# Optimization experiments

Hardware: AMD Instinct MI355X
Metric: run time of the kernel (lower is better)

Reference implementation:

```python
import jax, jax.numpy as jnp
import numpy as np

COMMITMENT_COST = 0.25
B, T, D = 32, 2048, 64
K = 1024


def setup_inputs() -> dict:
    key = jax.random.key(0)
    k1, k2 = jax.random.split(key)
    inputs = jax.random.normal(k1, (B, T, D), dtype=jnp.float32)
    # codebook init: uniform(-1/K, 1/K) in the original; use same scale
    embedding = jax.random.uniform(k2, (K, D), dtype=jnp.float32,
                                   minval=-1.0 / K, maxval=1.0 / K)
    return {"inputs": inputs, "embedding": embedding}


def reference(inputs, embedding):
    Bb, Tt, Dd = inputs.shape
    flat = inputs.reshape(-1, Dd)  # [N, D]
    dist = (jnp.sum(flat * flat, axis=1, keepdims=True)
            + jnp.sum(embedding * embedding, axis=1)[None, :]
            - 2.0 * (flat @ embedding.T))
    encoding_indices = jnp.argmin(dist, axis=1)  # [N]
    quantized = embedding[encoding_indices].reshape(Bb, Tt, Dd)
    # commitment loss: mse(stop_grad(quantized), inputs)
    e_latent_loss = jnp.mean((jax.lax.stop_gradient(quantized) - inputs) ** 2)
    vq_loss = COMMITMENT_COST * e_latent_loss
    codebook_loss = jnp.zeros((), dtype=jnp.float32)
    # straight-through estimator
    quantized_st = inputs + jax.lax.stop_gradient(quantized - inputs)
    return (quantized_st, encoding_indices.reshape(Bb, Tt),
            vq_loss, e_latent_loss, codebook_loss)
```

## Files before the change

kernel.cpp:

```cpp
#include <hip/hip_runtime.h>
#include <hip/hip_bf16.h>
#include <math.h>


typedef __attribute__((ext_vector_type(8))) short bf16x8;
typedef __attribute__((ext_vector_type(4))) float f32x4;

namespace {
constexpr int NROWS  = 65536;
constexpr int DDIM   = 64;
constexpr int KCODES = 1024;
constexpr float EPSB = 4e-5f;

constexpr size_t WS_LOSS = 0;
constexpr size_t WS_CNT  = 64;
constexpr size_t WS_SE   = 256;
constexpr size_t WS_EHB  = 8192;
constexpr size_t WS_ELB  = WS_EHB + (size_t)65536 * 2;
constexpr size_t WS_BIDX = WS_ELB + (size_t)65536 * 2;
constexpr size_t WS_LIST = WS_BIDX + (size_t)NROWS * 4;
constexpr size_t WS_KEY  = WS_LIST + (size_t)NROWS * 4;
constexpr size_t WS_MV   = WS_KEY + (size_t)NROWS * 8;
constexpr size_t WS_KV   = WS_MV + (size_t)4 * NROWS * 8;
}

__device__ inline short f2bf(float v) {
  __hip_bfloat16 h = __float2bfloat16(v);
  return *reinterpret_cast<short*>(&h);
}
__device__ inline float bf2f(short s) {
  __hip_bfloat16 h;
  *reinterpret_cast<short*>(&h) = s;
  return __bfloat162float(h);
}
__device__ inline f32x4 mfma16(bf16x8 a, bf16x8 b, f32x4 c) {
  return __builtin_amdgcn_mfma_f32_16x16x32_bf16(a, b, c, 0, 0, 0);
}
__device__ inline unsigned int fflip(unsigned int b) {
  return b ^ ((unsigned int)((int)b >> 31) | 0x80000000u);
}

__global__ __launch_bounds__(256) void vq_prep(const float* __restrict__ emb,
                                               float* __restrict__ se,
                                               short* __restrict__ ehB,
                                               short* __restrict__ elB,
                                               unsigned long long* __restrict__ keyBest,
                                               double* __restrict__ loss_accum,
                                               int* __restrict__ cnt) {
  #pragma clang fp contract(off)
  const int gid = blockIdx.x * 256 + (int)threadIdx.x;
  if (gid == 0) { *loss_accum = 0.0; *cnt = 0; }
  keyBest[gid] = ~0ull;

  if (gid < KCODES) {
    const float* e = emb + (size_t)gid * DDIM;
    float r[8];
    #pragma unroll
    for (int j = 0; j < 8; ++j) r[j] = e[j] * e[j];
    #pragma unroll
    for (int i = 8; i < DDIM; i += 8) {
      #pragma unroll
      for (int j = 0; j < 8; ++j) r[j] += e[i + j] * e[i + j];
    }
    se[gid] = ((r[0] + r[1]) + (r[2] + r[3])) + ((r[4] + r[5]) + (r[6] + r[7]));
  }

  if (gid < 8192) {
    const int t  = gid >> 7;
    const int dc = (gid >> 6) & 1;
    const int l  = gid & 63;
    const int code = t * 16 + (l & 15);
    const int d0   = dc * 32 + (l >> 4) * 8;
    const float* ep = emb + (size_t)code * DDIM + d0;
    const size_t ob = ((size_t)(t * 2 + dc) * 64 + l) * 8;
    #pragma unroll
    for (int i = 0; i < 8; ++i) {
      const float v = ep[i];
      const short h = f2bf(v);
      ehB[ob + i] = h;
      elB[ob + i] = f2bf(v - bf2f(h));
    }
  }
}

__global__ __launch_bounds__(256, 2) void vq_fused(const float* __restrict__ x,
                                                   const short* __restrict__ ehB,
                                                   const short* __restrict__ elB,
                                                   const float* __restrict__ se,
                                                   float2* __restrict__ mv,
                                                   unsigned long long* __restrict__ kv) {
  #pragma clang fp contract(off)
  __shared__ float sel[256];
  const int tid  = (int)threadIdx.x;
  const int l    = tid & 63;
  const int wid  = tid >> 6;
  const int quar = (int)blockIdx.x & 3;
  const int rblk = (int)blockIdx.x >> 2;
  const int t0   = quar * 16;
  sel[tid] = se[t0 * 16 + tid];
  __syncthreads();

  const int wrb = rblk * 128 + wid * 32;
  bf16x8 xh[2][2], xl[2][2];
  #pragma unroll
  for (int rt = 0; rt < 2; ++rt) {
    const float* xp = x + (size_t)(wrb + rt * 16 + (l & 15)) * DDIM + (l >> 4) * 8;
    #pragma unroll
    for (int dc = 0; dc < 2; ++dc) {
      const float4 v0 = *reinterpret_cast<const float4*>(xp + dc * 32);
      const float4 v1 = *reinterpret_cast<const float4*>(xp + dc * 32 + 4);
      const float vv[8] = {v0.x, v0.y, v0.z, v0.w, v1.x, v1.y, v1.z, v1.w};
      #pragma unroll
      for (int i = 0; i < 8; ++i) {
        const short h = f2bf(vv[i]);
        xh[rt][dc][i] = h;
        xl[rt][dc][i] = f2bf(vv[i] - bf2f(h));
      }
    }
  }

  float m1v[2][4], m2v[2][4];
  int   m1t[2][4];
  #pragma unroll
  for (int rt = 0; rt < 2; ++rt)
    #pragma unroll
    for (int r = 0; r < 4; ++r) { m1v[rt][r] = INFINITY; m2v[rt][r] = INFINITY; m1t[rt][r] = 0; }

  const size_t lb = (size_t)l * 8;
#define FRAGLD(buf, tt, half2) \
  (*reinterpret_cast<const bf16x8*>((buf) + (size_t)(tt) * 1024 + (half2) * 512 + lb))

  bf16x8 c0 = FRAGLD(ehB, t0, 0), c1 = FRAGLD(ehB, t0, 1),
         c2 = FRAGLD(elB, t0, 0), c3 = FRAGLD(elB, t0, 1);
  bf16x8 n0 = FRAGLD(ehB, t0 + 1, 0), n1 = FRAGLD(ehB, t0 + 1, 1),
         n2 = FRAGLD(elB, t0 + 1, 0), n3 = FRAGLD(elB, t0 + 1, 1);

  const f32x4 kz = {0.f, 0.f, 0.f, 0.f};
  #pragma unroll 4
  for (int tt = 0; tt < 16; ++tt) {
    const int t = t0 + tt;
    const int tf = (tt + 2 < 16) ? t + 2 : t0 + 15;
    bf16x8 f0 = FRAGLD(ehB, tf, 0), f1 = FRAGLD(ehB, tf, 1),
           f2 = FRAGLD(elB, tf, 0), f3 = FRAGLD(elB, tf, 1);

    f32x4 a0, a1;
    a0 = mfma16(xh[0][0], c0, kz);  a1 = mfma16(xh[1][0], c0, kz);
    a0 = mfma16(xh[0][1], c1, a0);  a1 = mfma16(xh[1][1], c1, a1);
    a0 = mfma16(xh[0][0], c2, a0);  a1 = mfma16(xh[1][0], c2, a1);
    a0 = mfma16(xh[0][1], c3, a0);  a1 = mfma16(xh[1][1], c3, a1);
    a0 = mfma16(xl[0][0], c0, a0);  a1 = mfma16(xl[1][0], c0, a1);
    a0 = mfma16(xl[0][1], c1, a0);  a1 = mfma16(xl[1][1], c1, a1);

    const float sev = sel[tt * 16 + (l & 15)];
    #pragma unroll
    for (int r = 0; r < 4; ++r) {
      {
        const float d = __builtin_fmaf(-2.0f, a0[r], sev);
        const bool c = d < m1v[0][r];
        m2v[0][r] = fminf(m2v[0][r], fmaxf(m1v[0][r], d));
        m1t[0][r] = c ? t : m1t[0][r];
        m1v[0][r] = fminf(m1v[0][r], d);
      }
      {
        const float d = __builtin_fmaf(-2.0f, a1[r], sev);
        const bool c = d < m1v[1][r];
        m2v[1][r] = fminf(m2v[1][r], fmaxf(m1v[1][r], d));
        m1t[1][r] = c ? t : m1t[1][r];
        m1v[1][r] = fminf(m1v[1][r], d);
      }
    }
    c0 = n0; c1 = n1; c2 = n2; c3 = n3;
    n0 = f0; n1 = f1; n2 = f2; n3 = f3;
  }
#undef FRAGLD

  const int colbase = l & 15;
  #pragma unroll
  for (int rt = 0; rt < 2; ++rt) {
    #pragma unroll
    for (int r = 0; r < 4; ++r) {
      float m1 = m1v[rt][r], m2 = m2v[rt][r];
      unsigned long long key =
          ((unsigned long long)fflip(__float_as_uint(m1)) << 32)
          | (unsigned)(m1t[rt][r] * 16 + colbase);
      #pragma unroll
      for (int off = 1; off < 16; off <<= 1) {
        const unsigned long long ok = __shfl_xor(key, off, 16);
        const float om1 = __shfl_xor(m1, off, 16);
        const float om2 = __shfl_xor(m2, off, 16);
        m2 = fminf(fminf(m2, om2), fmaxf(m1, om1));
        m1 = fminf(m1, om1);
        key = (ok < key) ? ok : key;
      }
      if (colbase == 0) {
        const int row = wrb + rt * 16 + (l >> 4) * 4 + r;
        mv[(size_t)quar * NROWS + row] = make_float2(m1, m2);
        kv[(size_t)quar * NROWS + row] = key;
      }
    }
  }
}

__global__ __launch_bounds__(256) void vq_combine(const float2* __restrict__ mv,
                                                  const unsigned long long* __restrict__ kv,
                                                  int* __restrict__ bidx,
                                                  int* __restrict__ list,
                                                  int* __restrict__ cnt) {
  const int gid = blockIdx.x * 256 + (int)threadIdx.x;
  const int l = (int)threadIdx.x & 63;
  const float2 A = mv[gid];
  const float2 B = mv[(size_t)NROWS + gid];
  const float2 C = mv[(size_t)2 * NROWS + gid];
  const float2 D = mv[(size_t)3 * NROWS + gid];
  unsigned long long kg = kv[gid];
  {
    unsigned long long k2 = kv[(size_t)NROWS + gid];     kg = (k2 < kg) ? k2 : kg;
    k2 = kv[(size_t)2 * NROWS + gid];                    kg = (k2 < kg) ? k2 : kg;
    k2 = kv[(size_t)3 * NROWS + gid];                    kg = (k2 < kg) ? k2 : kg;
  }
  const float lo1 = fminf(A.x, B.x), hi1 = fmaxf(A.x, B.x);
  const float lo2 = fminf(C.x, D.x), hi2 = fmaxf(C.x, D.x);
  const float m1g = fminf(lo1, lo2);
  const float sec = fminf(fmaxf(lo1, lo2), fminf(hi1, hi2));
  const float m2g = fminf(sec, fminf(fminf(A.y, B.y), fminf(C.y, D.y)));
  const bool cert = m2g > m1g + EPSB;
  bidx[gid] = cert ? (int)(kg & 0xffffffffull) : -1;

  const unsigned long long mask = __ballot(!cert);
  int base = 0;
  if (l == 0 && mask) base = atomicAdd(cnt, (int)__popcll(mask));
  base = __shfl(base, 0, 64);
  if (!cert) {
    const int off = (int)__popcll(mask & ((1ull << l) - 1ull));
    list[base + off] = gid;
  }
}

__global__ __launch_bounds__(64) void vq_exact(const float* __restrict__ x,
                                               const float* __restrict__ emb,
                                               const float* __restrict__ se,
                                               const int* __restrict__ list,
                                               const int* __restrict__ cnt,
                                               unsigned long long* __restrict__ keyBest) {
  #pragma clang fp contract(off)
  __shared__ __align__(16) float eL[32 * DDIM];
  const int n = *cnt;
  if (n == 0) return;
  const int nrb = (n + 63) >> 6;
  const int ntasks = nrb * 32;
  const int l = (int)threadIdx.x;

  for (int t = (int)blockIdx.x; t < ntasks; t += (int)gridDim.x) {
    const int part = t & 31;
    const int rb   = t >> 5;
    const int j0   = part * 32;

    {
      const float4* src = reinterpret_cast<const float4*>(emb + (size_t)j0 * DDIM);
      float4* dst = reinterpret_cast<float4*>(eL);
      #pragma unroll
      for (int i = 0; i < 8; ++i) dst[i * 64 + l] = src[i * 64 + l];
    }
    __syncthreads();

    const int idx = rb * 64 + l;
    const bool act = idx < n;
    const int row = act ? list[idx] : 0;
    const float4* xr4 = reinterpret_cast<const float4*>(x + (size_t)row * DDIM);

    float xv[DDIM];
    #pragma unroll
    for (int q = 0; q < 16; ++q) {
      const float4 v = xr4[q];
      xv[q * 4 + 0] = v.x; xv[q * 4 + 1] = v.y;
      xv[q * 4 + 2] = v.z; xv[q * 4 + 3] = v.w;
    }

    float rr[8];
    #pragma unroll
    for (int j = 0; j < 8; ++j) rr[j] = xv[j] * xv[j];
    #pragma unroll
    for (int i = 8; i < DDIM; i += 8) {
      #pragma unroll
      for (int j = 0; j < 8; ++j) rr[j] += xv[i + j] * xv[i + j];
    }
    const float sx = ((rr[0] + rr[1]) + (rr[2] + rr[3])) + ((rr[4] + rr[5]) + (rr[6] + rr[7]));

    unsigned long long best = ~0ull;
    #pragma unroll 1
    for (int g = 0; g < 8; ++g) {
      const int jb = g * 4;
      const float4* e0 = reinterpret_cast<const float4*>(eL + (jb + 0) * DDIM);
      const float4* e1 = reinterpret_cast<const float4*>(eL + (jb + 1) * DDIM);
      const float4* e2 = reinterpret_cast<const float4*>(eL + (jb + 2) * DDIM);
      const float4* e3 = reinterpret_cast<const float4*>(eL + (jb + 3) * DDIM);
      float a0 = 0.f, a1 = 0.f, a2 = 0.f, a3 = 0.f;
      #pragma unroll
      for (int q = 0; q < 16; ++q) {
        const float4 v0 = e0[q], v1 = e1[q], v2 = e2[q], v3 = e3[q];
        const float xa = xv[q * 4 + 0], xb = xv[q * 4 + 1];
        const float xc = xv[q * 4 + 2], xd = xv[q * 4 + 3];
        a0 = __builtin_fmaf(xa, v0.x, a0); a0 = __builtin_fmaf(xb, v0.y, a0);
        a0 = __builtin_fmaf(xc, v0.z, a0); a0 = __builtin_fmaf(xd, v0.w, a0);
        a1 = __builtin_fmaf(xa, v1.x, a1); a1 = __builtin_fmaf(xb, v1.y, a1);
        a1 = __builtin_fmaf(xc, v1.z, a1); a1 = __builtin_fmaf(xd, v1.w, a1);
        a2 = __builtin_fmaf(xa, v2.x, a2); a2 = __builtin_fmaf(xb, v2.y, a2);
        a2 = __builtin_fmaf(xc, v2.z, a2); a2 = __builtin_fmaf(xd, v2.w, a2);
        a3 = __builtin_fmaf(xa, v3.x, a3); a3 = __builtin_fmaf(xb, v3.y, a3);
        a3 = __builtin_fmaf(xc, v3.z, a3); a3 = __builtin_fmaf(xd, v3.w, a3);
      }
      const int j = j0 + jb;
      const float T0 = sx + se[j + 0];
      const float T1 = sx + se[j + 1];
      const float T2 = sx + se[j + 2];
      const float T3 = sx + se[j + 3];
      const float di0 = __builtin_fmaf(-2.0f, a0, T0);
      const float di1 = __builtin_fmaf(-2.0f, a1, T1);
      const float di2 = __builtin_fmaf(-2.0f, a2, T2);
      const float di3 = __builtin_fmaf(-2.0f, a3, T3);
      unsigned long long k;
      k = ((unsigned long long)fflip(__float_as_uint(di0)) << 32) | (unsigned)(j + 0);
      best = (k < best) ? k : best;
      k = ((unsigned long long)fflip(__float_as_uint(di1)) << 32) | (unsigned)(j + 1);
      best = (k < best) ? k : best;
      k = ((unsigned long long)fflip(__float_as_uint(di2)) << 32) | (unsigned)(j + 2);
      best = (k < best) ? k : best;
      k = ((unsigned long long)fflip(__float_as_uint(di3)) << 32) | (unsigned)(j + 3);
      best = (k < best) ? k : best;
    }
    if (act) atomicMin(&keyBest[row], best);
    __syncthreads();
  }
}

__global__ __launch_bounds__(256) void vq_finalize(const float* __restrict__ x,
                                                   const float* __restrict__ emb,
                                                   const int* __restrict__ bidx,
                                                   const unsigned long long* __restrict__ keyBest,
                                                   float* __restrict__ out,
                                                   double* __restrict__ loss_accum) {
  #pragma clang fp contract(off)
  __shared__ float wsum[4];
  const int tid = (int)threadIdx.x;
  const int l   = tid & 63;
  const int wid = tid >> 6;
  const int sub = l >> 4;
  const int q16 = l & 15;
  float lacc = 0.f;

  #pragma unroll
  for (int it = 0; it < 4; ++it) {
    const int row = blockIdx.x * 64 + it * 16 + wid * 4 + sub;
    int bi = bidx[row];
    if (bi < 0) bi = (int)(keyBest[row] & 0xffffffffull);
    const float4 xv = reinterpret_cast<const float4*>(x)[(size_t)row * 16 + q16];
    const float4 ev = reinterpret_cast<const float4*>(emb)[(size_t)bi * 16 + q16];
    const float da = ev.x - xv.x;
    const float db = ev.y - xv.y;
    const float dc = ev.z - xv.z;
    const float dd = ev.w - xv.w;
    float4 o;
    o.x = xv.x + da; o.y = xv.y + db; o.z = xv.z + dc; o.w = xv.w + dd;
    reinterpret_cast<float4*>(out)[(size_t)row * 16 + q16] = o;
    lacc += da * da + db * db + dc * dc + dd * dd;
    if (q16 == 0) out[(size_t)NROWS * DDIM + row] = (float)bi;
  }
  #pragma unroll
  for (int off = 32; off > 0; off >>= 1) lacc += __shfl_down(lacc, off, 64);
  if (l == 0) wsum[wid] = lacc;
  __syncthreads();
  if (tid == 0)
    atomicAdd(loss_accum, (double)(wsum[0] + wsum[1] + wsum[2] + wsum[3]));
}

__global__ void vq_scalars(const double* __restrict__ loss_accum,
                           float* __restrict__ out) {
  if (threadIdx.x == 0 && blockIdx.x == 0) {
    const double mm = *loss_accum / (double)((size_t)NROWS * DDIM);
    const float el = (float)mm;
    float* tail = out + (size_t)NROWS * DDIM + NROWS;
    tail[0] = 0.25f * el;
    tail[1] = el;
    tail[2] = 0.0f;
  }
}

extern "C" void kernel_launch(void* const* d_in, const int* in_sizes, int n_in,
                              void* d_out, int out_size, void* d_ws, size_t ws_size,
                              hipStream_t stream) {
  const float* x   = (const float*)d_in[0];
  const float* emb = (const float*)d_in[1];
  float* out = (float*)d_out;
  char* ws = (char*)d_ws;

  double* loss_accum = (double*)(ws + WS_LOSS);
  int*    cnt        = (int*)(ws + WS_CNT);
  float*  se         = (float*)(ws + WS_SE);
  short*  ehB        = (short*)(ws + WS_EHB);
  short*  elB        = (short*)(ws + WS_ELB);
  int*    bidx       = (int*)(ws + WS_BIDX);
  int*    list       = (int*)(ws + WS_LIST);
  unsigned long long* keyBest = (unsigned long long*)(ws + WS_KEY);
  float2* mv         = (float2*)(ws + WS_MV);
  unsigned long long* kv = (unsigned long long*)(ws + WS_KV);

  vq_prep<<<NROWS / 256, 256, 0, stream>>>(emb, se, ehB, elB, keyBest,
                                           loss_accum, cnt);
  vq_fused<<<(NROWS / 128) * 4, 256, 0, stream>>>(x, ehB, elB, se, mv, kv);
  vq_combine<<<NROWS / 256, 256, 0, stream>>>(mv, kv, bidx, list, cnt);
  vq_exact<<<2048, 64, 0, stream>>>(x, emb, se, list, cnt, keyBest);
  vq_finalize<<<NROWS / 64, 256, 0, stream>>>(x, emb, bidx, keyBest, out,
                                              loss_accum);
  vq_scalars<<<1, 64, 0, stream>>>(loss_accum, out);
}
```

Before: 98.73 us.

## Fuse output write into combine kernel; finalize only uncertain rows

The combine kernel now writes the quantized output, index and loss contribution for every row whose approximate argmin is certain, keeping the decisions in shared memory instead of a global bidx array. A small final kernel then processes only the rows listed as uncertain, using the exact-pass result. This removes a full pass that reread x and bidx for all rows, and moves most output writing earlier, before the exact pass. In exchange, the combine kernel becomes heavier and its loop now branches per row on the certainty flag.

```diff
diff --git a/kernel.cpp b/kernel.cpp
--- a/kernel.cpp
+++ b/kernel.cpp
@@ -201,39 +201,79 @@
   }
 }
 
-__global__ __launch_bounds__(256) void vq_combine(const float2* __restrict__ mv,
-                                                  const unsigned long long* __restrict__ kv,
-                                                  int* __restrict__ bidx,
-                                                  int* __restrict__ list,
-                                                  int* __restrict__ cnt) {
-  const int gid = blockIdx.x * 256 + (int)threadIdx.x;
-  const int l = (int)threadIdx.x & 63;
-  const float2 A = mv[gid];
-  const float2 B = mv[(size_t)NROWS + gid];
-  const float2 C = mv[(size_t)2 * NROWS + gid];
-  const float2 D = mv[(size_t)3 * NROWS + gid];
-  unsigned long long kg = kv[gid];
+__global__ __launch_bounds__(256) void vq_combine_out(const float2* __restrict__ mv,
+                                                      const unsigned long long* __restrict__ kv,
+                                                      const float* __restrict__ x,
+                                                      const float* __restrict__ emb,
+                                                      int* __restrict__ list,
+                                                      int* __restrict__ cnt,
+                                                      float* __restrict__ out,
+                                                      double* __restrict__ loss_accum) {
+  #pragma clang fp contract(off)
+  __shared__ int   sbidx[256];
+  __shared__ float wsum[4];
+  const int tid = (int)threadIdx.x;
+  const int gid = blockIdx.x * 256 + tid;
+  const int l   = tid & 63;
+
   {
-    unsigned long long k2 = kv[(size_t)NROWS + gid];     kg = (k2 < kg) ? k2 : kg;
-    k2 = kv[(size_t)2 * NROWS + gid];                    kg = (k2 < kg) ? k2 : kg;
-    k2 = kv[(size_t)3 * NROWS + gid];                    kg = (k2 < kg) ? k2 : kg;
-  }
-  const float lo1 = fminf(A.x, B.x), hi1 = fmaxf(A.x, B.x);
-  const float lo2 = fminf(C.x, D.x), hi2 = fmaxf(C.x, D.x);
-  const float m1g = fminf(lo1, lo2);
-  const float sec = fminf(fmaxf(lo1, lo2), fminf(hi1, hi2));
-  const float m2g = fminf(sec, fminf(fminf(A.y, B.y), fminf(C.y, D.y)));
-  const bool cert = m2g > m1g + EPSB;
-  bidx[gid] = cert ? (int)(kg & 0xffffffffull) : -1;
-
-  const unsigned long long mask = __ballot(!cert);
-  int base = 0;
-  if (l == 0 && mask) base = atomicAdd(cnt, (int)__popcll(mask));
-  base = __shfl(base, 0, 64);
-  if (!cert) {
-    const int off = (int)__popcll(mask & ((1ull << l) - 1ull));
-    list[base + off] = gid;
-  }
+    const float2 A = mv[gid];
+    const float2 B = mv[(size_t)NROWS + gid];
+    const float2 C = mv[(size_t)2 * NROWS + gid];
+    const float2 D = mv[(size_t)3 * NROWS + gid];
+    unsigned long long kg = kv[gid];
+    {
+      unsigned long long k2 = kv[(size_t)NROWS + gid];     kg = (k2 < kg) ? k2 : kg;
+      k2 = kv[(size_t)2 * NROWS + gid];                    kg = (k2 < kg) ? k2 : kg;
+      k2 = kv[(size_t)3 * NROWS + gid];                    kg = (k2 < kg) ? k2 : kg;
+    }
+    const float lo1 = fminf(A.x, B.x), hi1 = fmaxf(A.x, B.x);
+    const float lo2 = fminf(C.x, D.x), hi2 = fmaxf(C.x, D.x);
+    const float m1g = fminf(lo1, lo2);
+    const float sec = fminf(fmaxf(lo1, lo2), fminf(hi1, hi2));
+    const float m2g = fminf(sec, fminf(fminf(A.y, B.y), fminf(C.y, D.y)));
+    const bool cert = m2g > m1g + EPSB;
+    sbidx[tid] = cert ? (int)(kg & 0xffffffffull) : -1;
+
+    const unsigned long long mask = __ballot(!cert);
+    int base = 0;
+    if (l == 0 && mask) base = atomicAdd(cnt, (int)__popcll(mask));
+    base = __shfl(base, 0, 64);
+    if (!cert) {
+      const int off = (int)__popcll(mask & ((1ull << l) - 1ull));
+      list[base + off] = gid;
+    }
+  }
+  __syncthreads();
+
+  const int wid = tid >> 6;
+  const int sub = l >> 4;
+  const int q16 = l & 15;
+  float lacc = 0.f;
+
+  for (int it = 0; it < 16; ++it) {
+    const int rloc = it * 16 + wid * 4 + sub;
+    const int bi = sbidx[rloc];
+    if (bi < 0) continue;
+    const int row = blockIdx.x * 256 + rloc;
+    const float4 xv = reinterpret_cast<const float4*>(x)[(size_t)row * 16 + q16];
+    const float4 ev = reinterpret_cast<const float4*>(emb)[(size_t)bi * 16 + q16];
+    const float da = ev.x - xv.x;
+    const float db = ev.y - xv.y;
+    const float dc = ev.z - xv.z;
+    const float dd = ev.w - xv.w;
+    float4 o;
+    o.x = xv.x + da; o.y = xv.y + db; o.z = xv.z + dc; o.w = xv.w + dd;
+    reinterpret_cast<float4*>(out)[(size_t)row * 16 + q16] = o;
+    lacc += da * da + db * db + dc * dc + dd * dd;
+    if (q16 == 0) out[(size_t)NROWS * DDIM + row] = (float)bi;
+  }
+  #pragma unroll
+  for (int off = 32; off > 0; off >>= 1) lacc += __shfl_down(lacc, off, 64);
+  if (l == 0) wsum[wid] = lacc;
+  __syncthreads();
+  if (tid == 0)
+    atomicAdd(loss_accum, (double)(wsum[0] + wsum[1] + wsum[2] + wsum[3]));
 }
 
 __global__ __launch_bounds__(64) void vq_exact(const float* __restrict__ x,
@@ -333,26 +373,27 @@
   }
 }
 
-__global__ __launch_bounds__(256) void vq_finalize(const float* __restrict__ x,
-                                                   const float* __restrict__ emb,
-                                                   const int* __restrict__ bidx,
-                                                   const unsigned long long* __restrict__ keyBest,
-                                                   float* __restrict__ out,
-                                                   double* __restrict__ loss_accum) {
+__global__ __launch_bounds__(256) void vq_minifinal(const float* __restrict__ x,
+                                                    const float* __restrict__ emb,
+                                                    const int* __restrict__ list,
+                                                    const int* __restrict__ cnt,
+                                                    const unsigned long long* __restrict__ keyBest,
+                                                    float* __restrict__ out,
+                                                    double* __restrict__ loss_accum) {
   #pragma clang fp contract(off)
-  __shared__ float wsum[4];
-  const int tid = (int)threadIdx.x;
-  const int l   = tid & 63;
-  const int wid = tid >> 6;
+  const int n = *cnt;
+  const int l   = (int)threadIdx.x & 63;
   const int sub = l >> 4;
   const int q16 = l & 15;
+  const int w   = blockIdx.x * 4 + ((int)threadIdx.x >> 6);
+  const int nW  = (int)gridDim.x * 4;
   float lacc = 0.f;
 
-  #pragma unroll
-  for (int it = 0; it < 4; ++it) {
-    const int row = blockIdx.x * 64 + it * 16 + wid * 4 + sub;
-    int bi = bidx[row];
-    if (bi < 0) bi = (int)(keyBest[row] & 0xffffffffull);
+  for (int base = w * 4; base < n; base += nW * 4) {
+    const int i = base + sub;
+    if (i >= n) continue;
+    const int row = list[i];
+    const int bi = (int)(keyBest[row] & 0xffffffffull);
     const float4 xv = reinterpret_cast<const float4*>(x)[(size_t)row * 16 + q16];
     const float4 ev = reinterpret_cast<const float4*>(emb)[(size_t)bi * 16 + q16];
     const float da = ev.x - xv.x;
@@ -367,10 +408,7 @@
   }
   #pragma unroll
   for (int off = 32; off > 0; off >>= 1) lacc += __shfl_down(lacc, off, 64);
-  if (l == 0) wsum[wid] = lacc;
-  __syncthreads();
-  if (tid == 0)
-    atomicAdd(loss_accum, (double)(wsum[0] + wsum[1] + wsum[2] + wsum[3]));
+  if (l == 0 && lacc != 0.f) atomicAdd(loss_accum, (double)lacc);
 }
 
 __global__ void vq_scalars(const double* __restrict__ loss_accum,
@@ -398,7 +436,6 @@
   float*  se         = (float*)(ws + WS_SE);
   short*  ehB        = (short*)(ws + WS_EHB);
   short*  elB        = (short*)(ws + WS_ELB);
-  int*    bidx       = (int*)(ws + WS_BIDX);
   int*    list       = (int*)(ws + WS_LIST);
   unsigned long long* keyBest = (unsigned long long*)(ws + WS_KEY);
   float2* mv         = (float2*)(ws + WS_MV);
@@ -407,9 +444,10 @@
   vq_prep<<<NROWS / 256, 256, 0, stream>>>(emb, se, ehB, elB, keyBest,
                                            loss_accum, cnt);
   vq_fused<<<(NROWS / 128) * 4, 256, 0, stream>>>(x, ehB, elB, se, mv, kv);
-  vq_combine<<<NROWS / 256, 256, 0, stream>>>(mv, kv, bidx, list, cnt);
+  vq_combine_out<<<NROWS / 256, 256, 0, stream>>>(mv, kv, x, emb, list, cnt,
+                                                  out, loss_accum);
   vq_exact<<<2048, 64, 0, stream>>>(x, emb, se, list, cnt, keyBest);
-  vq_finalize<<<NROWS / 64, 256, 0, stream>>>(x, emb, bidx, keyBest, out,
-                                              loss_accum);
+  vq_minifinal<<<256, 256, 0, stream>>>(x, emb, list, cnt, keyBest, out,
+                                        loss_accum);
   vq_scalars<<<1, 64, 0, stream>>>(loss_accum, out);
 }
```

After: 94.13 us (median of 2 runs). 4.7% less time.
